# Optimization experiments

Measured on AMD Instinct MI355X. Metric: run time of the kernel, lower is better.

Reference implementation:

```python
import jax, jax.numpy as jnp
import numpy as np

CHEB_K = 2  # Chebyshev polynomial order (init arg cheb_k)


def _avwgcn(x, E, w_pool, b_pool):
    """Adaptive Vertex-Wise Graph Convolution (AGCRN's AVWGCN).
    x: [B, N, C_in], E: [N, D], w_pool: [D, K, C_in, C_out], b_pool: [D, C_out].
    """
    N = E.shape[0]
    # adaptive adjacency from node embeddings
    supports = jax.nn.softmax(jax.nn.relu(E @ E.T), axis=1)  # [N, N]
    support_set = [jnp.eye(N, dtype=x.dtype), supports]
    for _ in range(2, CHEB_K):
        support_set.append(2.0 * supports @ support_set[-1] - support_set[-2])
    supports_k = jnp.stack(support_set)  # [K, N, N]
    # per-node adaptive weights/bias generated from embeddings
    weights = jnp.einsum('nd,dkio->nkio', E, w_pool)  # [N, K, C_in, C_out]
    bias = E @ b_pool  # [N, C_out]
    # graph propagation then per-node adaptive projection
    x_g = jnp.einsum('knm,bmc->bnkc', supports_k, x)  # [B, N, K, C_in]
    return jnp.einsum('bnki,nkio->bno', x_g, weights) + bias  # [B, N, C_out]


def setup_inputs() -> dict:
    key = jax.random.key(0)
    ks = jax.random.split(key, 7)
    B, N, DIN, DOUT, D = 64, 2048, 2, 64, 10
    return {
        'x': jax.random.normal(ks[0], (B, N, DIN), dtype=jnp.float32),
        'state': jax.random.normal(ks[1], (B, N, DOUT), dtype=jnp.float32),
        'node_embeddings': jax.random.normal(ks[2], (N, D), dtype=jnp.float32),
        'gate_w_pool': jax.random.normal(ks[3], (D, CHEB_K, DIN + DOUT, 2 * DOUT), dtype=jnp.float32) * 0.1,
        'gate_b_pool': jax.random.normal(ks[4], (D, 2 * DOUT), dtype=jnp.float32) * 0.1,
        'update_w_pool': jax.random.normal(ks[5], (D, CHEB_K, DIN + DOUT, DOUT), dtype=jnp.float32) * 0.1,
        'update_b_pool': jax.random.normal(ks[6], (D, DOUT), dtype=jnp.float32) * 0.1,
    }


def reference(x, state, node_embeddings, gate_w_pool, gate_b_pool, update_w_pool, update_b_pool):
    hidden_dim = state.shape[-1]
    input_and_state = jnp.concatenate([x, state], axis=-1)  # [B, N, DIN+DOUT]
    z_r = jax.nn.sigmoid(_avwgcn(input_and_state, node_embeddings, gate_w_pool, gate_b_pool))
    z, r = z_r[..., :hidden_dim], z_r[..., hidden_dim:]
    candidate = jnp.concatenate([x, z * state], axis=-1)
    hc = jnp.tanh(_avwgcn(candidate, node_embeddings, update_w_pool, update_b_pool))
    h = r * state + (1.0 - r) * hc
    return h
```

## Files before the change

kernel.cpp:

```cpp
#include <hip/hip_runtime.h>
#include <math.h>

#define N_NODES 2048
#define BATCH   64
#define DIN     2
#define DOUT    64
#define CIN     66
#define CP      68
#define D_EMB   10
#define GOUT    128
#define NCOLS   (BATCH*CP)
#define MK      2048
#define KPAD    136
#define INP     160
#define WHALF   20480
#define WBLOB   40960

typedef __attribute__((ext_vector_type(8))) short bf16x8;
typedef __attribute__((ext_vector_type(8))) unsigned short u16x8;
typedef __attribute__((ext_vector_type(4))) float f32x4;

__device__ __forceinline__ unsigned short f2bf_rn(float f) {
    unsigned u = __builtin_bit_cast(unsigned, f);
    unsigned r = u + 0x7FFFu + ((u >> 16) & 1u);
    return (unsigned short)(r >> 16);
}
__device__ __forceinline__ float bf2f(unsigned short h) {
    unsigned u = ((unsigned)h) << 16;
    return __builtin_bit_cast(float, u);
}

__device__ __forceinline__ void gload_lds16(const void* g, void* l) {
    __builtin_amdgcn_global_load_lds(
        (const __attribute__((address_space(1))) unsigned int*)g,
        (__attribute__((address_space(3))) unsigned int*)l, 16, 0, 0);
}

__device__ __forceinline__ int frag_addr(int strip, int kt, int row, int slice) {
    const int byte = ((strip * 5 + kt) * 16 + row) * 64 + slice * 16;
    return byte ^ ((row & 7) << 4);
}

__global__ __launch_bounds__(256) void transpose_pool_kernel(
    const float* __restrict__ wp, float* __restrict__ wpT, int OC, int total)
{
    const int idx = blockIdx.x * 256 + threadIdx.x;
    if (idx >= total) return;
    const int kp   = idx % KPAD;
    const int rest = idx / KPAD;
    const int o    = rest % OC;
    const int d    = rest / OC;
    wpT[idx] = (kp < 132) ? wp[((size_t)d * 132 + kp) * OC + o] : 0.f;
}

__global__ __launch_bounds__(256) void supports_kernel(
    const float* __restrict__ E, unsigned short* __restrict__ S_hi)
{
    const int n   = blockIdx.x;
    const int tid = threadIdx.x;

    float en[D_EMB];
#pragma unroll
    for (int d = 0; d < D_EMB; ++d) en[d] = E[n * D_EMB + d];

    float vals[8];
    float mx = -1e30f;
#pragma unroll
    for (int j = 0; j < 8; ++j) {
        const int m = tid + j * 256;
        float dot = 0.f;
#pragma unroll
        for (int d = 0; d < D_EMB; ++d) dot += en[d] * E[m * D_EMB + d];
        dot = fmaxf(dot, 0.f);
        vals[j] = dot;
        mx = fmaxf(mx, dot);
    }

    __shared__ float sred[4];
    for (int off = 32; off > 0; off >>= 1) mx = fmaxf(mx, __shfl_xor(mx, off));
    if ((tid & 63) == 0) sred[tid >> 6] = mx;
    __syncthreads();
    mx = fmaxf(fmaxf(sred[0], sred[1]), fmaxf(sred[2], sred[3]));

    float sum = 0.f;
#pragma unroll
    for (int j = 0; j < 8; ++j) { vals[j] = __expf(vals[j] - mx); sum += vals[j]; }

    __syncthreads();
    for (int off = 32; off > 0; off >>= 1) sum += __shfl_xor(sum, off);
    if ((tid & 63) == 0) sred[tid >> 6] = sum;
    __syncthreads();
    sum = sred[0] + sred[1] + sred[2] + sred[3];

    const float inv = 1.f / sum;
#pragma unroll
    for (int j = 0; j < 8; ++j)
        S_hi[(size_t)n * N_NODES + tid + j * 256] = f2bf_rn(vals[j] * inv);
}

__global__ __launch_bounds__(256) void zero_tail_kernel(unsigned short* __restrict__ IN)
{
    const int idx = blockIdx.x * 256 + threadIdx.x;
    if (idx >= N_NODES * BATCH * 13) return;
    const int row = idx / 13, j = idx % 13;
    *(unsigned int*)((char*)IN + (size_t)row * INP * 2 + 268 + j * 4) = 0u;
}

__global__ __launch_bounds__(256) void build_xt_kernel(
    const float* __restrict__ x, const float* __restrict__ state,
    const unsigned short* __restrict__ INz, const int use_zs,
    unsigned short* __restrict__ XT)
{
    const int b   = blockIdx.y;
    const int m0  = blockIdx.x * 64;
    const int tid = threadIdx.x;
    __shared__ float T[64][69];

    {
        const int r = tid >> 2;
        const int q = (tid & 3) * 16;
        if (use_zs) {
            const unsigned int* p = (const unsigned int*)
                ((const char*)INz + (((size_t)(m0 + r) * BATCH + b) * INP + 2 + q) * 2);
#pragma unroll
            for (int t = 0; t < 8; ++t) {
                const unsigned int v = p[t];
                T[r][DIN + q + 2 * t]     = bf2f((unsigned short)(v & 0xFFFFu));
                T[r][DIN + q + 2 * t + 1] = bf2f((unsigned short)(v >> 16));
            }
        } else {
#pragma unroll
            for (int u = 0; u < 4; ++u) {
                const float4 v = *(const float4*)&state[((size_t)b * N_NODES + m0 + r) * DOUT + q + u * 4];
                T[r][DIN + q + u * 4 + 0] = v.x;
                T[r][DIN + q + u * 4 + 1] = v.y;
                T[r][DIN + q + u * 4 + 2] = v.z;
                T[r][DIN + q + u * 4 + 3] = v.w;
            }
        }
    }
    if (tid < 128) {
        const int r = tid >> 1, c = tid & 1;
        T[r][c] = x[((size_t)b * N_NODES + m0 + r) * DIN + c];
        T[r][CIN + c] = 0.f;
    }
    __syncthreads();

    for (int idx = tid; idx < CP * 64; idx += 256) {
        const int c  = idx >> 6;
        const int mm = idx & 63;
        XT[((size_t)(b * CP + c)) * N_NODES + m0 + mm] = f2bf_rn(T[mm][c]);
    }
}

__global__ __launch_bounds__(256) void gemm_mfma_kernel(
    const unsigned short* __restrict__ A,
    const unsigned short* __restrict__ BT, unsigned short* __restrict__ INout)
{
    __shared__ __align__(16) unsigned short As[4096];
    __shared__ __align__(16) unsigned short Bs[4096];

    const int tid  = threadIdx.x;
    const int lane = tid & 63;
    const int w    = tid >> 6;
    const int wr   = w >> 1, wc = w & 1;

    const int wg   = blockIdx.x;
    const int wgid = (wg & 7) * 68 + (wg >> 3);
    const int bn   = wgid % 34;
    const int bm   = wgid / 34;

    f32x4 acc[4][4];
#pragma unroll
    for (int i = 0; i < 4; ++i)
#pragma unroll
        for (int j = 0; j < 4; ++j) acc[i][j] = (f32x4){0.f, 0.f, 0.f, 0.f};

    const int srow = ((tid >> 6) << 4) + (tid & 15);
    const int scol = ((tid >> 4) & 3) * 8;
    const unsigned a_off0 = (unsigned)(bm * 128 + srow) * MK + scol;
    const unsigned a_off1 = a_off0 + 64u * MK;
    const unsigned b_off0 = (unsigned)(bn * 128 + srow) * MK + scol;
    const unsigned b_off1 = b_off0 + 64u * MK;

    unsigned short* asl0 = As + tid * 8;
    unsigned short* asl1 = As + 2048 + tid * 8;
    unsigned short* bsl0 = Bs + tid * 8;
    unsigned short* bsl1 = Bs + 2048 + tid * 8;

#pragma unroll 1
    for (int k0 = 0; k0 < MK; k0 += 32) {
        gload_lds16(A  + a_off0 + k0, asl0);
        gload_lds16(A  + a_off1 + k0, asl1);
        gload_lds16(BT + b_off0 + k0, bsl0);
        gload_lds16(BT + b_off1 + k0, bsl1);
        __syncthreads();

        bf16x8 af[4], bf[4];
#pragma unroll
        for (int i = 0; i < 4; ++i)
            af[i] = *(const bf16x8*)(As + ((wr * 4 + i) * 64 + lane) * 8);
#pragma unroll
        for (int j = 0; j < 4; ++j)
            bf[j] = *(const bf16x8*)(Bs + ((wc * 4 + j) * 64 + lane) * 8);
#pragma unroll
        for (int i = 0; i < 4; ++i)
#pragma unroll
            for (int j = 0; j < 4; ++j)
                acc[i][j] = __builtin_amdgcn_mfma_f32_16x16x32_bf16(
                    af[i], bf[j], acc[i][j], 0, 0, 0);
        __syncthreads();
    }

    const int crow0 = bm * 128 + wr * 64;
    const int ccol0 = bn * 128 + wc * 64;
#pragma unroll
    for (int j = 0; j < 4; ++j) {
        const int col = ccol0 + j * 16 + (lane & 15);
        const int b   = col / 68;
        const int c   = col - b * 68;
#pragma unroll
        for (int i = 0; i < 4; ++i)
#pragma unroll
            for (int r = 0; r < 4; ++r) {
                const int row = crow0 + i * 16 + (lane >> 4) * 4 + r;
                INout[((size_t)row * BATCH + b) * INP + 66 + c] = f2bf_rn(acc[i][j][r]);
            }
    }
}

__global__ __launch_bounds__(256) void wgen_kernel(
    const float* __restrict__ E, const float* __restrict__ wpT,
    unsigned char* __restrict__ Wc, int n0, int NH, int OC)
{
    const int tid  = threadIdx.x;
    const int cid  = blockIdx.x * 256 + tid;
    const int half = cid / 1280;
    const int rest = cid % 1280;
    const int o_l  = rest / 20;
    const int s    = rest % 20;
    const int o_g  = half * 64 + o_l;

    __shared__ float en_s[16][D_EMB];
    if (tid < 16 * D_EMB) {
        const int i = tid / D_EMB, d = tid % D_EMB;
        en_s[i][d] = E[(n0 + blockIdx.y * 16 + i) * D_EMB + d];
    }

    float wv[D_EMB][8];
    if (s < 17) {
        const float* p = wpT + (size_t)o_g * KPAD + s * 8;
#pragma unroll
        for (int d = 0; d < D_EMB; ++d) {
            const float4 a = *(const float4*)(p + (size_t)d * OC * KPAD);
            const float4 b = *(const float4*)(p + (size_t)d * OC * KPAD + 4);
            wv[d][0] = a.x; wv[d][1] = a.y; wv[d][2] = a.z; wv[d][3] = a.w;
            wv[d][4] = b.x; wv[d][5] = b.y; wv[d][6] = b.z; wv[d][7] = b.w;
        }
    } else {
#pragma unroll
        for (int d = 0; d < D_EMB; ++d)
#pragma unroll
            for (int u = 0; u < 8; ++u) wv[d][u] = 0.f;
    }
    __syncthreads();

    const int addr = frag_addr(o_l >> 4, s >> 2, o_l & 15, s & 3);
    unsigned char* base0 = Wc + (size_t)blockIdx.y * 16 * NH * WBLOB + (size_t)half * WBLOB;
#pragma unroll 1
    for (int i = 0; i < 16; ++i) {
        float v[8] = {0.f, 0.f, 0.f, 0.f, 0.f, 0.f, 0.f, 0.f};
#pragma unroll
        for (int d = 0; d < D_EMB; ++d) {
            const float e = en_s[i][d];
#pragma unroll
            for (int u = 0; u < 8; ++u) v[u] += e * wv[d][u];
        }
        u16x8 hv, lv;
#pragma unroll
        for (int u = 0; u < 8; ++u) {
            const unsigned short h = f2bf_rn(v[u]);
            hv[u] = h;
            lv[u] = f2bf_rn(v[u] - bf2f(h));
        }
        unsigned char* nb = base0 + (size_t)i * NH * WBLOB;
        *(u16x8*)(nb + addr)         = hv;
        *(u16x8*)(nb + WHALF + addr) = lv;
    }
}

union afrag { u16x8 u; bf16x8 s; };

__global__ __launch_bounds__(256) void gate_mfma_kernel(
    const float* __restrict__ E, const float* __restrict__ bp,
    const float* __restrict__ x, const float* __restrict__ state,
    unsigned short* __restrict__ IN, const unsigned char* __restrict__ Wc,
    int n0, unsigned short* __restrict__ Rb)
{
    const int n_l  = blockIdx.x;
    const int n    = n0 + n_l;
    const int half = blockIdx.y;
    const int tid  = threadIdx.x;

    __shared__ __align__(16) unsigned char Ws[WBLOB];
    __shared__ float bias_l[64];

    const unsigned char* src = Wc + (size_t)n_l * (2 * WBLOB) + (size_t)half * WBLOB;
#pragma unroll
    for (int i = 0; i < 10; ++i)
        gload_lds16(src + (tid + i * 256) * 16, Ws + (tid + i * 256) * 16);

    if (tid < 64) {
        float s = 0.f;
#pragma unroll
        for (int d = 0; d < D_EMB; ++d)
            s += E[n * D_EMB + d] * bp[d * GOUT + half * 64 + tid];
        bias_l[tid] = s;
    }

    const int lane = tid & 63, w = tid >> 6;
    const int row = lane & 15, sl = lane >> 4;
    const int b = w * 16 + row;
    const float* stp = state + ((size_t)b * N_NODES + n) * DOUT;
    const float2 xv  = *(const float2*)(x + ((size_t)b * N_NODES + n) * DIN);
    const unsigned short* inr = IN + ((size_t)n * BATCH + b) * INP;

    afrag af[5];
    {
        float f[8];
        if (sl == 0) {
            f[0] = xv.x; f[1] = xv.y;
            const float2 s0 = *(const float2*)(stp + 0);
            const float2 s1 = *(const float2*)(stp + 2);
            const float2 s2 = *(const float2*)(stp + 4);
            f[2] = s0.x; f[3] = s0.y; f[4] = s1.x; f[5] = s1.y; f[6] = s2.x; f[7] = s2.y;
        } else {
            const float* sp = stp + sl * 8 - 2;
#pragma unroll
            for (int t = 0; t < 4; ++t) {
                const float2 v = *(const float2*)(sp + 2 * t);
                f[2 * t] = v.x; f[2 * t + 1] = v.y;
            }
        }
#pragma unroll
        for (int u = 0; u < 8; ++u) af[0].u[u] = f2bf_rn(f[u]);
    }
    {
        const float* sp = stp + 30 + sl * 8;
        float f[8];
#pragma unroll
        for (int t = 0; t < 4; ++t) {
            const float2 v = *(const float2*)(sp + 2 * t);
            f[2 * t] = v.x; f[2 * t + 1] = v.y;
        }
#pragma unroll
        for (int u = 0; u < 8; ++u) af[1].u[u] = f2bf_rn(f[u]);
    }
    if (sl == 0) {
        af[2].u[0] = f2bf_rn(stp[62]);
        af[2].u[1] = f2bf_rn(stp[63]);
        const unsigned int* q = (const unsigned int*)((const char*)inr + 132);
        const unsigned int q0 = q[0], q1 = q[1], q2 = q[2];
        af[2].u[2] = (unsigned short)q0; af[2].u[3] = (unsigned short)(q0 >> 16);
        af[2].u[4] = (unsigned short)q1; af[2].u[5] = (unsigned short)(q1 >> 16);
        af[2].u[6] = (unsigned short)q2; af[2].u[7] = (unsigned short)(q2 >> 16);
    } else {
        af[2].u = *(const u16x8*)(inr + 64 + sl * 8);
    }
    af[3].u = *(const u16x8*)(inr + 96 + sl * 8);
    af[4].u = *(const u16x8*)(inr + 128 + sl * 8);

    __syncthreads();

    f32x4 acc[4];
#pragma unroll
    for (int j = 0; j < 4; ++j) acc[j] = (f32x4){0.f, 0.f, 0.f, 0.f};
#pragma unroll
    for (int j = 0; j < 4; ++j) {
#pragma unroll
        for (int kt = 0; kt < 5; ++kt) {
            const bf16x8 bh = *(const bf16x8*)(Ws + frag_addr(j, kt, row, sl));
            acc[j] = __builtin_amdgcn_mfma_f32_16x16x32_bf16(af[kt].s, bh, acc[j], 0, 0, 0);
        }
#pragma unroll
        for (int kt = 0; kt < 5; ++kt) {
            const bf16x8 bl = *(const bf16x8*)(Ws + WHALF + frag_addr(j, kt, row, sl));
            acc[j] = __builtin_amdgcn_mfma_f32_16x16x32_bf16(af[kt].s, bl, acc[j], 0, 0, 0);
        }
    }

#pragma unroll
    for (int j = 0; j < 4; ++j) {
        const int o_l = j * 16 + row;
        const float bs = bias_l[o_l];
#pragma unroll
        for (int r = 0; r < 4; ++r) {
            const int bb = w * 16 + sl * 4 + r;
            const float sg = 1.f / (1.f + __expf(-(acc[j][r] + bs)));
            if (half == 0) {
                const float st = state[((size_t)bb * N_NODES + n) * DOUT + o_l];
                IN[((size_t)n * BATCH + bb) * INP + 2 + o_l] = f2bf_rn(sg * st);
            } else {
                Rb[((size_t)n * BATCH + bb) * DOUT + o_l] = f2bf_rn(sg);
            }
        }
    }
}

__global__ __launch_bounds__(256) void update_mfma_kernel(
    const float* __restrict__ E, const float* __restrict__ bp,
    const float* __restrict__ x, const float* __restrict__ state,
    const unsigned short* __restrict__ IN, const unsigned char* __restrict__ Wc,
    int n0, const unsigned short* __restrict__ Rb, float* __restrict__ out)
{
    const int n_l = blockIdx.x;
    const int n   = n0 + n_l;
    const int tid = threadIdx.x;

    __shared__ __align__(16) unsigned char Ws[WBLOB];
    __shared__ float bias_l[64];

    const unsigned char* src = Wc + (size_t)n_l * WBLOB;
#pragma unroll
    for (int i = 0; i < 10; ++i)
        gload_lds16(src + (tid + i * 256) * 16, Ws + (tid + i * 256) * 16);

    if (tid < 64) {
        float s = 0.f;
#pragma unroll
        for (int d = 0; d < D_EMB; ++d)
            s += E[n * D_EMB + d] * bp[d * DOUT + tid];
        bias_l[tid] = s;
    }

    const int lane = tid & 63, w = tid >> 6;
    const int row = lane & 15, sl = lane >> 4;
    const int b = w * 16 + row;
    const unsigned short* inr = IN + ((size_t)n * BATCH + b) * INP;

    afrag af[5];
    if (sl == 0) {
        const float2 xv = *(const float2*)(x + ((size_t)b * N_NODES + n) * DIN);
        af[0].u[0] = f2bf_rn(xv.x);
        af[0].u[1] = f2bf_rn(xv.y);
        const unsigned int* q = (const unsigned int*)((const char*)inr + 4);
        const unsigned int q0 = q[0], q1 = q[1], q2 = q[2];
        af[0].u[2] = (unsigned short)q0; af[0].u[3] = (unsigned short)(q0 >> 16);
        af[0].u[4] = (unsigned short)q1; af[0].u[5] = (unsigned short)(q1 >> 16);
        af[0].u[6] = (unsigned short)q2; af[0].u[7] = (unsigned short)(q2 >> 16);
    } else {
        af[0].u = *(const u16x8*)(inr + sl * 8);
    }
#pragma unroll
    for (int kt = 1; kt < 5; ++kt)
        af[kt].u = *(const u16x8*)(inr + kt * 32 + sl * 8);

    __syncthreads();

    f32x4 acc[4];
#pragma unroll
    for (int j = 0; j < 4; ++j) acc[j] = (f32x4){0.f, 0.f, 0.f, 0.f};
#pragma unroll
    for (int j = 0; j < 4; ++j) {
#pragma unroll
        for (int kt = 0; kt < 5; ++kt) {
            const bf16x8 bh = *(const bf16x8*)(Ws + frag_addr(j, kt, row, sl));
            acc[j] = __builtin_amdgcn_mfma_f32_16x16x32_bf16(af[kt].s, bh, acc[j], 0, 0, 0);
        }
#pragma unroll
        for (int kt = 0; kt < 5; ++kt) {
            const bf16x8 bl = *(const bf16x8*)(Ws + WHALF + frag_addr(j, kt, row, sl));
            acc[j] = __builtin_amdgcn_mfma_f32_16x16x32_bf16(af[kt].s, bl, acc[j], 0, 0, 0);
        }
    }

#pragma unroll
    for (int j = 0; j < 4; ++j) {
        const int o_l = j * 16 + row;
        const float bs = bias_l[o_l];
#pragma unroll
        for (int r = 0; r < 4; ++r) {
            const int bb = w * 16 + sl * 4 + r;
            const float hc = tanhf(acc[j][r] + bs);
            const float rr = bf2f(Rb[((size_t)n * BATCH + bb) * DOUT + o_l]);
            const float st = state[((size_t)bb * N_NODES + n) * DOUT + o_l];
            out[((size_t)bb * N_NODES + n) * DOUT + o_l] = rr * st + (1.f - rr) * hc;
        }
    }
}

extern "C" void kernel_launch(void* const* d_in, const int* in_sizes, int n_in,
                              void* d_out, int out_size, void* d_ws, size_t ws_size,
                              hipStream_t stream)
{
    const float* x  = (const float*)d_in[0];
    const float* st = (const float*)d_in[1];
    const float* E  = (const float*)d_in[2];
    const float* gw = (const float*)d_in[3];
    const float* gb = (const float*)d_in[4];
    const float* uw = (const float*)d_in[5];
    const float* ub = (const float*)d_in[6];
    float* out = (float*)d_out;

    unsigned char* ws = (unsigned char*)d_ws;
    unsigned short* S_hi = (unsigned short*)ws;
    unsigned short* XT   = (unsigned short*)(ws + 8388608);
    unsigned short* IN   = (unsigned short*)(ws + 26214400);
    unsigned short* Rb   = (unsigned short*)(ws + 68157440);
    float* wpTg          = (float*)(ws + 84934656);
    float* wpTu          = (float*)(ws + 85630976);
    unsigned char* Wc    = ws + 85979136;

    const size_t fixed_b = 85979136;
    int C = 64;
    const int cands[5] = {2048, 1024, 512, 256, 128};
    for (int i = 0; i < 5; ++i) {
        if (ws_size >= fixed_b + (size_t)cands[i] * (2 * WBLOB)) { C = cands[i]; break; }
    }
    const int nch = N_NODES / C;

    const int tg = D_EMB * GOUT * KPAD;
    const int tu = D_EMB * DOUT * KPAD;
    transpose_pool_kernel<<<(tg + 255) / 256, 256, 0, stream>>>(gw, wpTg, GOUT, tg);
    transpose_pool_kernel<<<(tu + 255) / 256, 256, 0, stream>>>(uw, wpTu, DOUT, tu);

    supports_kernel<<<N_NODES, 256, 0, stream>>>(E, S_hi);
    zero_tail_kernel<<<(N_NODES * BATCH * 13 + 255) / 256, 256, 0, stream>>>(IN);
    build_xt_kernel<<<dim3(N_NODES / 64, BATCH), 256, 0, stream>>>(x, st, IN, 0, XT);
    gemm_mfma_kernel<<<544, 256, 0, stream>>>(S_hi, XT, IN);

    for (int ch = 0; ch < nch; ++ch) {
        const int n0 = ch * C;
        wgen_kernel<<<dim3(10, C / 16), 256, 0, stream>>>(E, wpTg, Wc, n0, 2, GOUT);
        gate_mfma_kernel<<<dim3(C, 2), 256, 0, stream>>>(E, gb, x, st, IN, Wc, n0, Rb);
    }

    build_xt_kernel<<<dim3(N_NODES / 64, BATCH), 256, 0, stream>>>(x, st, IN, 1, XT);
    gemm_mfma_kernel<<<544, 256, 0, stream>>>(S_hi, XT, IN);

    for (int ch = 0; ch < nch; ++ch) {
        const int n0 = ch * C;
        wgen_kernel<<<dim3(5, C / 16), 256, 0, stream>>>(E, wpTu, Wc, n0, 1, DOUT);
        update_mfma_kernel<<<C, 256, 0, stream>>>(E, ub, x, st, IN, Wc, n0, Rb, out);
    }
}
```

Baseline: 485.4 us.

## Double-buffer LDS tiles and use 8 waves in support GEMM

The support×X GEMM now uses 512 threads (8 waves, each computing a 32x64 sub-tile) and double-buffers the A/B LDS tiles. The next k-slice is prefetched while the current one runs through MFMA, which removes one barrier per iteration. The goal is to hide global-to-LDS latency and raise occupancy. In exchange it doubles LDS use and lowers MFMA work per wave, and this GEMM is only part of the total pipeline.

```diff
diff --git a/kernel.cpp b/kernel.cpp
--- a/kernel.cpp
+++ b/kernel.cpp
@@ -153,12 +153,12 @@
     }
 }
 
-__global__ __launch_bounds__(256) void gemm_mfma_kernel(
+__global__ __launch_bounds__(512) void gemm_mfma_kernel(
     const unsigned short* __restrict__ A,
     const unsigned short* __restrict__ BT, unsigned short* __restrict__ INout)
 {
-    __shared__ __align__(16) unsigned short As[4096];
-    __shared__ __align__(16) unsigned short Bs[4096];
+    __shared__ __align__(16) unsigned short As[2][4096];
+    __shared__ __align__(16) unsigned short Bs[2][4096];
 
     const int tid  = threadIdx.x;
     const int lane = tid & 63;
@@ -170,49 +170,62 @@
     const int bn   = wgid % 34;
     const int bm   = wgid / 34;
 
-    f32x4 acc[4][4];
-#pragma unroll
-    for (int i = 0; i < 4; ++i)
+    f32x4 acc[2][4];
+#pragma unroll
+    for (int i = 0; i < 2; ++i)
 #pragma unroll
         for (int j = 0; j < 4; ++j) acc[i][j] = (f32x4){0.f, 0.f, 0.f, 0.f};
 
     const int srow = ((tid >> 6) << 4) + (tid & 15);
     const int scol = ((tid >> 4) & 3) * 8;
-    const unsigned a_off0 = (unsigned)(bm * 128 + srow) * MK + scol;
-    const unsigned a_off1 = a_off0 + 64u * MK;
-    const unsigned b_off0 = (unsigned)(bn * 128 + srow) * MK + scol;
-    const unsigned b_off1 = b_off0 + 64u * MK;
-
-    unsigned short* asl0 = As + tid * 8;
-    unsigned short* asl1 = As + 2048 + tid * 8;
-    unsigned short* bsl0 = Bs + tid * 8;
-    unsigned short* bsl1 = Bs + 2048 + tid * 8;
-
+    const unsigned a_off = (unsigned)(bm * 128 + srow) * MK + scol;
+    const unsigned b_off = (unsigned)(bn * 128 + srow) * MK + scol;
+
+    gload_lds16(A  + a_off, &As[0][tid * 8]);
+    gload_lds16(BT + b_off, &Bs[0][tid * 8]);
+
+    int cur = 0;
 #pragma unroll 1
-    for (int k0 = 0; k0 < MK; k0 += 32) {
-        gload_lds16(A  + a_off0 + k0, asl0);
-        gload_lds16(A  + a_off1 + k0, asl1);
-        gload_lds16(BT + b_off0 + k0, bsl0);
-        gload_lds16(BT + b_off1 + k0, bsl1);
+    for (int k0 = 0; k0 < MK - 32; k0 += 32) {
         __syncthreads();
 
-        bf16x8 af[4], bf[4];
-#pragma unroll
-        for (int i = 0; i < 4; ++i)
-            af[i] = *(const bf16x8*)(As + ((wr * 4 + i) * 64 + lane) * 8);
+        gload_lds16(A  + a_off + k0 + 32, &As[cur ^ 1][tid * 8]);
+        gload_lds16(BT + b_off + k0 + 32, &Bs[cur ^ 1][tid * 8]);
+
+        bf16x8 af[2], bf[4];
+#pragma unroll
+        for (int i = 0; i < 2; ++i)
+            af[i] = *(const bf16x8*)(&As[cur][((wr * 2 + i) * 64 + lane) * 8]);
 #pragma unroll
         for (int j = 0; j < 4; ++j)
-            bf[j] = *(const bf16x8*)(Bs + ((wc * 4 + j) * 64 + lane) * 8);
-#pragma unroll
-        for (int i = 0; i < 4; ++i)
+            bf[j] = *(const bf16x8*)(&Bs[cur][((wc * 4 + j) * 64 + lane) * 8]);
+#pragma unroll
+        for (int i = 0; i < 2; ++i)
 #pragma unroll
             for (int j = 0; j < 4; ++j)
                 acc[i][j] = __builtin_amdgcn_mfma_f32_16x16x32_bf16(
                     af[i], bf[j], acc[i][j], 0, 0, 0);
-        __syncthreads();
-    }
-
-    const int crow0 = bm * 128 + wr * 64;
+        cur ^= 1;
+    }
+    __syncthreads();
+
+    {
+        bf16x8 af[2], bf[4];
+#pragma unroll
+        for (int i = 0; i < 2; ++i)
+            af[i] = *(const bf16x8*)(&As[cur][((wr * 2 + i) * 64 + lane) * 8]);
+#pragma unroll
+        for (int j = 0; j < 4; ++j)
+            bf[j] = *(const bf16x8*)(&Bs[cur][((wc * 4 + j) * 64 + lane) * 8]);
+#pragma unroll
+        for (int i = 0; i < 2; ++i)
+#pragma unroll
+            for (int j = 0; j < 4; ++j)
+                acc[i][j] = __builtin_amdgcn_mfma_f32_16x16x32_bf16(
+                    af[i], bf[j], acc[i][j], 0, 0, 0);
+    }
+
+    const int crow0 = bm * 128 + wr * 32;
     const int ccol0 = bn * 128 + wc * 64;
 #pragma unroll
     for (int j = 0; j < 4; ++j) {
@@ -220,7 +233,7 @@
         const int b   = col / 68;
         const int c   = col - b * 68;
 #pragma unroll
-        for (int i = 0; i < 4; ++i)
+        for (int i = 0; i < 2; ++i)
 #pragma unroll
             for (int r = 0; r < 4; ++r) {
                 const int row = crow0 + i * 16 + (lane >> 4) * 4 + r;
@@ -527,7 +540,7 @@
     supports_kernel<<<N_NODES, 256, 0, stream>>>(E, S_hi);
     zero_tail_kernel<<<(N_NODES * BATCH * 13 + 255) / 256, 256, 0, stream>>>(IN);
     build_xt_kernel<<<dim3(N_NODES / 64, BATCH), 256, 0, stream>>>(x, st, IN, 0, XT);
-    gemm_mfma_kernel<<<544, 256, 0, stream>>>(S_hi, XT, IN);
+    gemm_mfma_kernel<<<544, 512, 0, stream>>>(S_hi, XT, IN);
 
     for (int ch = 0; ch < nch; ++ch) {
         const int n0 = ch * C;
@@ -536,7 +549,7 @@
     }
 
     build_xt_kernel<<<dim3(N_NODES / 64, BATCH), 256, 0, stream>>>(x, st, IN, 1, XT);
-    gemm_mfma_kernel<<<544, 256, 0, stream>>>(S_hi, XT, IN);
+    gemm_mfma_kernel<<<544, 512, 0, stream>>>(S_hi, XT, IN);
 
     for (int ch = 0; ch < nch; ++ch) {
         const int n0 = ch * C;
```

Result: no change. 488.7 us (+0.7%).

## Triple-buffer LDS in support GEMM with async prefetch two tiles ahead

Applied to the files above, without the earlier changes.

The MFMA GEMM kernel now uses three LDS buffers for the A and B tiles and issues global-to-LDS loads two k-steps ahead. Explicit vmcnt waits and a single barrier per iteration replace the load-then-sync-compute-sync pattern. The goal is to hide global memory latency behind the MFMA work. This triples LDS use per block (48KB), which may lower occupancy, and it relies on the vmcnt accounting being correct.

```diff
diff --git a/kernel.cpp b/kernel.cpp
--- a/kernel.cpp
+++ b/kernel.cpp
@@ -11,6 +11,7 @@
 #define GOUT    128
 #define NCOLS   (BATCH*CP)
 #define MK      2048
+#define NT      (MK/32)
 #define KPAD    136
 #define INP     160
 #define WHALF   20480
@@ -157,8 +158,8 @@
     const unsigned short* __restrict__ A,
     const unsigned short* __restrict__ BT, unsigned short* __restrict__ INout)
 {
-    __shared__ __align__(16) unsigned short As[4096];
-    __shared__ __align__(16) unsigned short Bs[4096];
+    __shared__ __align__(16) unsigned short As[3][4096];
+    __shared__ __align__(16) unsigned short Bs[3][4096];
 
     const int tid  = threadIdx.x;
     const int lane = tid & 63;
@@ -183,34 +184,46 @@
     const unsigned b_off0 = (unsigned)(bn * 128 + srow) * MK + scol;
     const unsigned b_off1 = b_off0 + 64u * MK;
 
-    unsigned short* asl0 = As + tid * 8;
-    unsigned short* asl1 = As + 2048 + tid * 8;
-    unsigned short* bsl0 = Bs + tid * 8;
-    unsigned short* bsl1 = Bs + 2048 + tid * 8;
-
+#define STAGE(k0, bs)                                              \
+    do {                                                           \
+        gload_lds16(A  + a_off0 + (k0), &As[bs][tid * 8]);         \
+        gload_lds16(A  + a_off1 + (k0), &As[bs][2048 + tid * 8]);  \
+        gload_lds16(BT + b_off0 + (k0), &Bs[bs][tid * 8]);         \
+        gload_lds16(BT + b_off1 + (k0), &Bs[bs][2048 + tid * 8]);  \
+    } while (0)
+
+    STAGE(0, 0);
+    STAGE(32, 1);
+
+    int cur = 0;
 #pragma unroll 1
-    for (int k0 = 0; k0 < MK; k0 += 32) {
-        gload_lds16(A  + a_off0 + k0, asl0);
-        gload_lds16(A  + a_off1 + k0, asl1);
-        gload_lds16(BT + b_off0 + k0, bsl0);
-        gload_lds16(BT + b_off1 + k0, bsl1);
-        __syncthreads();
+    for (int i = 0; i < NT; ++i) {
+        if (i < NT - 1) asm volatile("s_waitcnt vmcnt(4)" ::: "memory");
+        else            asm volatile("s_waitcnt vmcnt(0)" ::: "memory");
+        __builtin_amdgcn_s_barrier();
+
+        if (i + 2 < NT) {
+            const int nb = (cur + 2 >= 3) ? cur - 1 : cur + 2;
+            STAGE((i + 2) * 32, nb);
+        }
 
         bf16x8 af[4], bf[4];
 #pragma unroll
-        for (int i = 0; i < 4; ++i)
-            af[i] = *(const bf16x8*)(As + ((wr * 4 + i) * 64 + lane) * 8);
+        for (int q = 0; q < 4; ++q)
+            af[q] = *(const bf16x8*)(&As[cur][((wr * 4 + q) * 64 + lane) * 8]);
 #pragma unroll
         for (int j = 0; j < 4; ++j)
-            bf[j] = *(const bf16x8*)(Bs + ((wc * 4 + j) * 64 + lane) * 8);
-#pragma unroll
-        for (int i = 0; i < 4; ++i)
+            bf[j] = *(const bf16x8*)(&Bs[cur][((wc * 4 + j) * 64 + lane) * 8]);
+#pragma unroll
+        for (int q = 0; q < 4; ++q)
 #pragma unroll
             for (int j = 0; j < 4; ++j)
-                acc[i][j] = __builtin_amdgcn_mfma_f32_16x16x32_bf16(
-                    af[i], bf[j], acc[i][j], 0, 0, 0);
-        __syncthreads();
-    }
+                acc[q][j] = __builtin_amdgcn_mfma_f32_16x16x32_bf16(
+                    af[q], bf[j], acc[q][j], 0, 0, 0);
+
+        cur = (cur + 1 >= 3) ? 0 : cur + 1;
+    }
+#undef STAGE
 
     const int crow0 = bm * 128 + wr * 64;
     const int ccol0 = bn * 128 + wc * 64;
@@ -220,11 +233,11 @@
         const int b   = col / 68;
         const int c   = col - b * 68;
 #pragma unroll
-        for (int i = 0; i < 4; ++i)
+        for (int q = 0; q < 4; ++q)
 #pragma unroll
             for (int r = 0; r < 4; ++r) {
-                const int row = crow0 + i * 16 + (lane >> 4) * 4 + r;
-                INout[((size_t)row * BATCH + b) * INP + 66 + c] = f2bf_rn(acc[i][j][r]);
+                const int row = crow0 + q * 16 + (lane >> 4) * 4 + r;
+                INout[((size_t)row * BATCH + b) * INP + 66 + c] = f2bf_rn(acc[q][j][r]);
             }
     }
 }
```

Result: no change. 488.7 us (+0.7%).
